# Optimization experiments

Hardware: AMD Instinct MI355X
Metric: run time of the kernel (lower is better)

## Reference

```python
import jax, jax.numpy as jnp
import numpy as np

N_NODES = 100000
N_EDGES = 1600000
D_IN = 256
D_OUT = 128


def _gcn_norm(edge_index, num_nodes):
    # Add self-loops and compute symmetric normalization D^-1/2 A D^-1/2 (PyG GCNConv default).
    src, dst = edge_index[0], edge_index[1]
    loop = jnp.arange(num_nodes, dtype=edge_index.dtype)
    src = jnp.concatenate([src, loop])
    dst = jnp.concatenate([dst, loop])
    deg = jax.ops.segment_sum(jnp.ones_like(dst, dtype=jnp.float32), dst, num_segments=num_nodes)
    dinv = jnp.where(deg > 0, jax.lax.rsqrt(jnp.maximum(deg, 1.0)), 0.0)
    norm = dinv[src] * dinv[dst]  # [E + N]
    return src, dst, norm


def _gcn_conv(x, W, b, src, dst, norm, num_nodes):
    h = x @ W  # [N, d_out] transform first (d_out <= d_in keeps message traffic low)
    msg = h[src] * norm[:, None]  # [E+N, d_out] gather + scale
    out = jax.ops.segment_sum(msg, dst, num_segments=num_nodes)  # scatter-add
    return out + b


def setup_inputs() -> dict:
    key = jax.random.key(0)
    ks = jax.random.split(key, 8)
    x = jax.random.normal(ks[0], (N_NODES, D_IN), dtype=jnp.float32)
    edge_index = jax.random.randint(ks[1], (2, N_EDGES), 0, N_NODES, dtype=jnp.int64)
    s = 0.05
    return {
        "x": x,
        "edge_index": edge_index,
        "W1": jax.random.normal(ks[2], (D_IN, D_OUT), dtype=jnp.float32) * s,
        "b1": jnp.zeros((D_OUT,), dtype=jnp.float32),
        "W_mu": jax.random.normal(ks[3], (D_OUT, D_OUT), dtype=jnp.float32) * s,
        "b_mu": jnp.zeros((D_OUT,), dtype=jnp.float32),
        "W_ls": jax.random.normal(ks[4], (D_OUT, D_OUT), dtype=jnp.float32) * s,
        "b_ls": jnp.zeros((D_OUT,), dtype=jnp.float32),
    }


def reference(x, edge_index, W1, b1, W_mu, b_mu, W_ls, b_ls):
    num_nodes = x.shape[0]
    src, dst, norm = _gcn_norm(edge_index, num_nodes)
    h = jax.nn.relu(_gcn_conv(x, W1, b1, src, dst, norm, num_nodes))
    mu = _gcn_conv(h, W_mu, b_mu, src, dst, norm, num_nodes)
    logstd = _gcn_conv(h, W_ls, b_ls, src, dst, norm, num_nodes)
    return (mu, logstd)
```

## Files before the change

kernel.cpp:

```cpp
#include <hip/hip_runtime.h>
#include <hip/hip_bf16.h>
#include <hip/hip_fp16.h>

typedef __attribute__((ext_vector_type(8))) short short8;
typedef __attribute__((ext_vector_type(8))) _Float16 f16x8;
typedef __attribute__((ext_vector_type(4))) float f32x4;

#define EPB 16384

__global__ __launch_bounds__(256) void k_lhist(const int* __restrict__ dst, int* __restrict__ histT,
                                               int nE, int nblk, int nbins) {
  __shared__ int c[1024];
  int tid = threadIdx.x;
  for (int i = tid; i < nbins; i += 256) c[i] = 0;
  __syncthreads();
  int blk = blockIdx.x;
  int e0 = blk * EPB;
  int e1 = min(nE, e0 + EPB);
  if (e1 - e0 == EPB) {
#pragma unroll
    for (int it = 0; it < EPB / 1024; ++it) {
      int4 d = *(const int4*)(dst + e0 + it * 1024 + tid * 4);
      atomicAdd(&c[d.x >> 7], 1);
      atomicAdd(&c[d.y >> 7], 1);
      atomicAdd(&c[d.z >> 7], 1);
      atomicAdd(&c[d.w >> 7], 1);
    }
  } else {
    for (int i = e0 + tid; i < e1; i += 256) atomicAdd(&c[dst[i] >> 7], 1);
  }
  __syncthreads();
  for (int i = tid; i < nbins; i += 256) histT[i * nblk + blk] = c[i];
}

__global__ __launch_bounds__(256) void k_lscatter(
    const int* __restrict__ src, const int* __restrict__ dst, const int* __restrict__ subPtr,
    int* __restrict__ binned, int nE, int nblk, int nbins) {
  __shared__ int cur[1024];
  int tid = threadIdx.x;
  int blk = blockIdx.x;
  for (int i = tid; i < nbins; i += 256) cur[i] = subPtr[i * nblk + blk];
  __syncthreads();
  int e0 = blk * EPB;
  int e1 = min(nE, e0 + EPB);
  if (e1 - e0 == EPB) {
#pragma unroll
    for (int it = 0; it < EPB / 1024; ++it) {
      int base = e0 + it * 1024 + tid * 4;
      int4 s = *(const int4*)(src + base);
      int4 d = *(const int4*)(dst + base);
      int p0 = atomicAdd(&cur[d.x >> 7], 1);
      int p1 = atomicAdd(&cur[d.y >> 7], 1);
      int p2 = atomicAdd(&cur[d.z >> 7], 1);
      int p3 = atomicAdd(&cur[d.w >> 7], 1);
      binned[p0] = s.x | ((d.x & 127) << 20);
      binned[p1] = s.y | ((d.y & 127) << 20);
      binned[p2] = s.z | ((d.z & 127) << 20);
      binned[p3] = s.w | ((d.w & 127) << 20);
    }
  } else {
    for (int i = e0 + tid; i < e1; i += 256) {
      int d = dst[i];
      int pos = atomicAdd(&cur[d >> 7], 1);
      binned[pos] = src[i] | ((d & 127) << 20);
    }
  }
}

__global__ __launch_bounds__(256) void k_bin_cnt(
    const int* __restrict__ binned, const int* __restrict__ subPtr,
    int* __restrict__ cnt, int nE, int nblk, int nbins, int n) {
  __shared__ int c128[128];
  int b = blockIdx.x;
  int tid = threadIdx.x;
  if (tid < 128) c128[tid] = 0;
  __syncthreads();
  int s0 = subPtr[b * nblk];
  int s1 = (b + 1 < nbins) ? subPtr[(b + 1) * nblk] : nE;
  for (int i = s0 + tid; i < s1; i += 256)
    atomicAdd(&c128[(binned[i] >> 20) & 127], 1);
  __syncthreads();
  if (tid < 128) {
    int idx = (b << 7) + tid;
    if (idx < n) cnt[idx] = c128[tid];
  }
}

__global__ __launch_bounds__(256) void k_bin_place(
    const int* __restrict__ binned, const int* __restrict__ subPtr,
    const int* __restrict__ rowptr, int* __restrict__ col, int nE, int nblk, int nbins, int n) {
  __shared__ int cur128[128];
  int b = blockIdx.x;
  int tid = threadIdx.x;
  if (tid < 128) {
    int idx = (b << 7) + tid;
    cur128[tid] = (idx < n) ? rowptr[idx] : 0;
  }
  __syncthreads();
  int s0 = subPtr[b * nblk];
  int s1 = (b + 1 < nbins) ? subPtr[(b + 1) * nblk] : nE;
  for (int i = s0 + tid; i < s1; i += 256) {
    int e = binned[i];
    int pos = atomicAdd(&cur128[(e >> 20) & 127], 1);
    col[pos] = e & 0xFFFFF;
  }
}


__global__ void k_blocksum(const int* __restrict__ cnt, int* __restrict__ bsum, int n) {
  __shared__ int red[256];
  int tid = threadIdx.x;
  int base = blockIdx.x * 1024 + tid * 4;
  int s = 0;
#pragma unroll
  for (int i = 0; i < 4; i++) { int idx = base + i; if (idx < n) s += cnt[idx]; }
  red[tid] = s;
  __syncthreads();
  for (int off = 128; off > 0; off >>= 1) {
    if (tid < off) red[tid] += red[tid + off];
    __syncthreads();
  }
  if (tid == 0) bsum[blockIdx.x] = red[0];
}

__global__ void k_scan_bsum(int* __restrict__ bsum, int nb) {
  __shared__ int s[128];
  int tid = threadIdx.x;
  int v = (tid < nb) ? bsum[tid] : 0;
  s[tid] = v;
  __syncthreads();
  for (int off = 1; off < 128; off <<= 1) {
    int t = (tid >= off) ? s[tid - off] : 0;
    __syncthreads();
    s[tid] += t;
    __syncthreads();
  }
  if (tid < nb) bsum[tid] = s[tid] - v;
}

__global__ void k_scan_final(const int* __restrict__ cnt, const int* __restrict__ bsum,
                             int* __restrict__ rowptr, float* __restrict__ dinv, int n) {
  __shared__ int tsum[256];
  int tid = threadIdx.x;
  int base = blockIdx.x * 1024 + tid * 4;
  int v[4]; int s = 0;
#pragma unroll
  for (int i = 0; i < 4; i++) { v[i] = (base + i < n) ? cnt[base + i] : 0; s += v[i]; }
  tsum[tid] = s;
  __syncthreads();
  for (int off = 1; off < 256; off <<= 1) {
    int t = (tid >= off) ? tsum[tid - off] : 0;
    __syncthreads();
    tsum[tid] += t;
    __syncthreads();
  }
  int run = bsum[blockIdx.x] + tsum[tid] - s;
#pragma unroll
  for (int i = 0; i < 4; i++) {
    int idx = base + i;
    if (idx < n) {
      rowptr[idx] = run;
      if (dinv) dinv[idx] = rsqrtf((float)(v[i] + 1));
      run += v[i];
    }
  }
}


__global__ void k_prep_w(const float* __restrict__ W1,
                         const float* __restrict__ Wmu, const float* __restrict__ Wls,
                         const float* __restrict__ bmu, const float* __restrict__ bls,
                         __half* __restrict__ W1T, __half* __restrict__ WcT,
                         float* __restrict__ bcat) {
  int i = blockIdx.x * blockDim.x + threadIdx.x;
  if (i < 128 * 256) {
    int n = i >> 8, k = i & 255;
    W1T[i] = __float2half(W1[k * 128 + n]);
  } else if (i < 2 * 128 * 256) {
    int j = i - 128 * 256;
    int n = j >> 7, k = j & 127;
    float f = (n < 128) ? Wmu[k * 128 + n] : Wls[k * 128 + (n - 128)];
    WcT[j] = __float2half(f);
  } else if (i < 2 * 128 * 256 + 256) {
    int n = i - 2 * 128 * 256;
    bcat[n] = (n < 128) ? bmu[n] : bls[n - 128];
  }
}


#define LP 40

template <int AFMT, int OFMT>
__global__ __launch_bounds__(256) void k_gemm_mfma(
    const void* __restrict__ Av, const __half* __restrict__ WT,
    const float* __restrict__ bias, void* __restrict__ out0, void* __restrict__ out1,
    int M, int K, int split_out) {
  __shared__ _Float16 As[128 * LP];
  __shared__ _Float16 Bs[128 * LP];

  const int tid = threadIdx.x;
  const int lane = tid & 63;
  const int wv = tid >> 6;
  const int wr = wv >> 1, wc = wv & 1;
  const int rsel = lane >> 4;
  const int rrow = lane & 15;
  const int row0 = blockIdx.x * 128;
  const int col0 = blockIdx.y * 128;

  f32x4 acc[4][4];
#pragma unroll
  for (int m = 0; m < 4; m++)
#pragma unroll
    for (int n = 0; n < 4; n++) acc[m][n] = (f32x4){0.f, 0.f, 0.f, 0.f};

  const int srow = tid >> 1;
  const int skh = (tid & 1) * 16;

  for (int k0 = 0; k0 < K; k0 += 32) {
    if (row0 + srow < M) {
      if (AFMT == 0) {
        const float* src = (const float*)Av + (size_t)(row0 + srow) * K + k0 + skh;
        float4 f0 = *(const float4*)(src);
        float4 f1 = *(const float4*)(src + 4);
        float4 f2 = *(const float4*)(src + 8);
        float4 f3 = *(const float4*)(src + 12);
        f16x8 v0, v1;
        v0[0]=(_Float16)f0.x; v0[1]=(_Float16)f0.y; v0[2]=(_Float16)f0.z; v0[3]=(_Float16)f0.w;
        v0[4]=(_Float16)f1.x; v0[5]=(_Float16)f1.y; v0[6]=(_Float16)f1.z; v0[7]=(_Float16)f1.w;
        v1[0]=(_Float16)f2.x; v1[1]=(_Float16)f2.y; v1[2]=(_Float16)f2.z; v1[3]=(_Float16)f2.w;
        v1[4]=(_Float16)f3.x; v1[5]=(_Float16)f3.y; v1[6]=(_Float16)f3.z; v1[7]=(_Float16)f3.w;
        *(f16x8*)&As[srow * LP + skh]     = v0;
        *(f16x8*)&As[srow * LP + skh + 8] = v1;
      } else {
        const _Float16* src = (const _Float16*)Av + (size_t)(row0 + srow) * K + k0 + skh;
        *(f16x8*)&As[srow * LP + skh]     = *(const f16x8*)src;
        *(f16x8*)&As[srow * LP + skh + 8] = *(const f16x8*)(src + 8);
      }
    } else {
      f16x8 z = (f16x8){0,0,0,0,0,0,0,0};
      *(f16x8*)&As[srow * LP + skh] = z; *(f16x8*)&As[srow * LP + skh + 8] = z;
    }
    {
      const _Float16* s = (const _Float16*)WT + (size_t)(col0 + srow) * K + k0 + skh;
      *(f16x8*)&Bs[srow * LP + skh]     = *(const f16x8*)s;
      *(f16x8*)&Bs[srow * LP + skh + 8] = *(const f16x8*)(s + 8);
    }
    __syncthreads();

    f16x8 fa[4], fb[4];
#pragma unroll
    for (int m = 0; m < 4; m++)
      fa[m] = *(f16x8*)&As[(wr * 64 + m * 16 + rrow) * LP + rsel * 8];
#pragma unroll
    for (int n = 0; n < 4; n++)
      fb[n] = *(f16x8*)&Bs[(wc * 64 + n * 16 + rrow) * LP + rsel * 8];
#pragma unroll
    for (int m = 0; m < 4; m++)
#pragma unroll
      for (int n = 0; n < 4; n++)
        acc[m][n] = __builtin_amdgcn_mfma_f32_16x16x32_f16(fa[m], fb[n], acc[m][n], 0, 0, 0);
    __syncthreads();
  }

#pragma unroll
  for (int n = 0; n < 4; n++) {
    int col = col0 + wc * 64 + n * 16 + rrow;
    float badd = bias ? bias[col] : 0.f;
    void* dstBase = out0;
    int c = col;
    if (split_out && c >= 128) { dstBase = out1; c -= 128; }
#pragma unroll
    for (int m = 0; m < 4; m++) {
      f32x4 v = acc[m][n];
#pragma unroll
      for (int r = 0; r < 4; r++) {
        int row = row0 + wr * 64 + m * 16 + rsel * 4 + r;
        if (row < M) {
          if (OFMT == 0)
            ((float*)dstBase)[(size_t)row * 128 + c] = v[r] + badd;
          else
            ((__half*)dstBase)[(size_t)row * 128 + c] = __float2half(v[r] + badd);
        }
      }
    }
  }
}


__global__ __launch_bounds__(256) void k_spmm_h(
    const __half* __restrict__ in, const int* __restrict__ rowptr,
    const int* __restrict__ cnt, const int* __restrict__ col,
    const float* __restrict__ dinv,
    const float* __restrict__ bias, __half* __restrict__ out,
    int n, int use_bias, int relu_out) {
  int node = blockIdx.x * 4 + (threadIdx.x >> 6);
  if (node >= n) return;
  int lane = threadIdx.x & 63;

  const __half2* inp = (const __half2*)in;
  float di = dinv[node];
  float2 v = __half22float2(inp[(size_t)node * 64 + lane]);
  float accx = di * v.x;
  float accy = di * v.y;

  int beg = rowptr[node];
  int m = cnt[node];
  int i = 0;
  for (; i + 8 <= m; i += 8) {
    int c[8];
#pragma unroll
    for (int j = 0; j < 8; j++) c[j] = col[beg + i + j];
    float e[8];
#pragma unroll
    for (int j = 0; j < 8; j++) e[j] = dinv[c[j]];
    float2 u[8];
#pragma unroll
    for (int j = 0; j < 8; j++) u[j] = __half22float2(inp[(size_t)c[j] * 64 + lane]);
#pragma unroll
    for (int j = 0; j < 8; j++) { accx += e[j] * u[j].x; accy += e[j] * u[j].y; }
  }
  if (i < m) {
    int c[8];
#pragma unroll
    for (int j = 0; j < 8; j++) c[j] = col[(i + j < m) ? (beg + i + j) : beg];
    float e[8];
#pragma unroll
    for (int j = 0; j < 8; j++) e[j] = (i + j < m) ? dinv[c[j]] : 0.f;
    float2 u[8];
#pragma unroll
    for (int j = 0; j < 8; j++) u[j] = __half22float2(inp[(size_t)c[j] * 64 + lane]);
#pragma unroll
    for (int j = 0; j < 8; j++) { accx += e[j] * u[j].x; accy += e[j] * u[j].y; }
  }
  accx *= di;
  accy *= di;
  if (use_bias) {
    accx += bias[2 * lane];
    accy += bias[2 * lane + 1];
  }
  if (relu_out) {
    accx = fmaxf(accx, 0.f);
    accy = fmaxf(accy, 0.f);
  }
  ((__half2*)(out + (size_t)node * 128))[lane] = __floats2half2_rn(accx, accy);
}


__global__ __launch_bounds__(256) void k_spmm_gemm(
    const __half* __restrict__ in, const int* __restrict__ rowptr,
    const int* __restrict__ cnt, const int* __restrict__ col,
    const float* __restrict__ dinv,
    const __half* __restrict__ WcT, const float* __restrict__ bcat,
    float* __restrict__ out0, float* __restrict__ out1, int n) {
  __shared__ _Float16 gt[16 * 128];
  const int tid = threadIdx.x;
  const int lane = tid & 63;
  const int w = tid >> 6;
  const __half2* inp = (const __half2*)in;

  for (int q = 0; q < 4; q++) {
    int li = w * 4 + q;
    int node = blockIdx.x * 16 + li;
    float accx = 0.f, accy = 0.f;
    if (node < n) {
      float di = dinv[node];
      float2 v = __half22float2(inp[(size_t)node * 64 + lane]);
      accx = di * v.x;
      accy = di * v.y;
      int beg = rowptr[node];
      int m = cnt[node];
      int i = 0;
      for (; i + 8 <= m; i += 8) {
        int c[8];
#pragma unroll
        for (int j = 0; j < 8; j++) c[j] = col[beg + i + j];
        float e[8];
#pragma unroll
        for (int j = 0; j < 8; j++) e[j] = dinv[c[j]];
        float2 u[8];
#pragma unroll
        for (int j = 0; j < 8; j++) u[j] = __half22float2(inp[(size_t)c[j] * 64 + lane]);
#pragma unroll
        for (int j = 0; j < 8; j++) { accx += e[j] * u[j].x; accy += e[j] * u[j].y; }
      }
      if (i < m) {
        int c[8];
#pragma unroll
        for (int j = 0; j < 8; j++) c[j] = col[(i + j < m) ? (beg + i + j) : beg];
        float e[8];
#pragma unroll
        for (int j = 0; j < 8; j++) e[j] = (i + j < m) ? dinv[c[j]] : 0.f;
        float2 u[8];
#pragma unroll
        for (int j = 0; j < 8; j++) u[j] = __half22float2(inp[(size_t)c[j] * 64 + lane]);
#pragma unroll
        for (int j = 0; j < 8; j++) { accx += e[j] * u[j].x; accy += e[j] * u[j].y; }
      }
      accx *= di;
      accy *= di;
    }
    int slot = (lane >> 2) ^ (li & 7);
    *(__half2*)((char*)gt + li * 256 + slot * 16 + (lane & 3) * 4) =
        __floats2half2_rn(accx, accy);
  }
  __syncthreads();

  const int lr = lane & 15;
  const int lk = lane >> 4;
  f16x8 a[4];
#pragma unroll
  for (int ks = 0; ks < 4; ks++) {
    int slot = (ks * 4 + lk) ^ (lr & 7);
    a[ks] = *(const f16x8*)((const char*)gt + lr * 256 + slot * 16);
  }
#pragma unroll
  for (int ct = 0; ct < 4; ct++) {
    int colg = (w * 4 + ct) * 16 + lr;
    f32x4 acc = (f32x4){0.f, 0.f, 0.f, 0.f};
#pragma unroll
    for (int ks = 0; ks < 4; ks++) {
      f16x8 b = *(const f16x8*)((const _Float16*)WcT + (size_t)colg * 128 + ks * 32 + lk * 8);
      acc = __builtin_amdgcn_mfma_f32_16x16x32_f16(a[ks], b, acc, 0, 0, 0);
    }
    float badd = bcat[colg];
    float* dst = out0;
    int c = colg;
    if (c >= 128) { dst = out1; c -= 128; }
#pragma unroll
    for (int r = 0; r < 4; r++) {
      int node = blockIdx.x * 16 + lk * 4 + r;
      if (node < n) dst[(size_t)node * 128 + c] = acc[r] + badd;
    }
  }
}


extern "C" void kernel_launch(void* const* d_in, const int* in_sizes, int n_in,
                              void* d_out, int out_size, void* d_ws, size_t ws_size,
                              hipStream_t stream) {
  const float* x   = (const float*)d_in[0];
  const int*   ei  = (const int*)d_in[1];
  const float* W1  = (const float*)d_in[2];
  const float* b1  = (const float*)d_in[3];
  const float* Wmu = (const float*)d_in[4];
  const float* bmu = (const float*)d_in[5];
  const float* Wls = (const float*)d_in[6];
  const float* bls = (const float*)d_in[7];

  int N = in_sizes[0] / 256;
  int E = in_sizes[1] / 2;
  const int* src = ei;
  const int* dst = ei + E;

  int NBINS = (N + 127) >> 7;
  int NBLK  = (E + EPB - 1) / EPB;
  int NS    = NBINS * NBLK;

  char* ws = (char*)d_ws;
  size_t o = 0;
  auto alloc = [&](size_t b) { size_t c = o; o = (o + b + 511) & ~(size_t)511; return c; };
  int*   cnt     = (int*)(ws + alloc((size_t)N * 4));
  int*   rowptr  = (int*)(ws + alloc((size_t)N * 4));
  float* dinv    = (float*)(ws + alloc((size_t)N * 4));
  int*   bsum    = (int*)(ws + alloc(512));
  int*   histT   = (int*)(ws + alloc((size_t)NS * 4));
  int*   subPtr  = (int*)(ws + alloc((size_t)NS * 4));
  int*   col     = (int*)(ws + alloc((size_t)E * 4));
  int*   binned  = (int*)(ws + alloc((size_t)E * 4));
  __half* W1T  = (__half*)(ws + alloc(128 * 256 * 2));
  __half* WcT  = (__half*)(ws + alloc(256 * 128 * 2));
  float*  bcat = (float*)(ws + alloc(256 * 4));
  __half* h0   = (__half*)(ws + alloc((size_t)N * 128 * 2));
  __half* hBuf = (__half*)(ws + alloc((size_t)N * 128 * 2));

  float* outMu = (float*)d_out;
  float* outLs = outMu + (size_t)N * 128;

  int nbScanN = (N + 1023) / 1024;
  int nbScanS = (NS + 1023) / 1024;

  k_lhist<<<NBLK, 256, 0, stream>>>(dst, histT, E, NBLK, NBINS);
  k_blocksum<<<nbScanS, 256, 0, stream>>>(histT, bsum, NS);
  k_scan_bsum<<<1, 128, 0, stream>>>(bsum, nbScanS);
  k_scan_final<<<nbScanS, 256, 0, stream>>>(histT, bsum, subPtr, nullptr, NS);
  k_lscatter<<<NBLK, 256, 0, stream>>>(src, dst, subPtr, binned, E, NBLK, NBINS);
  k_bin_cnt<<<NBINS, 256, 0, stream>>>(binned, subPtr, cnt, E, NBLK, NBINS, N);
  k_blocksum<<<nbScanN, 256, 0, stream>>>(cnt, bsum, N);
  k_scan_bsum<<<1, 128, 0, stream>>>(bsum, nbScanN);
  k_scan_final<<<nbScanN, 256, 0, stream>>>(cnt, bsum, rowptr, dinv, N);
  k_bin_place<<<NBINS, 256, 0, stream>>>(binned, subPtr, rowptr, col, E, NBLK, NBINS, N);

  k_prep_w<<<(2 * 128 * 256 + 256 + 255) / 256, 256, 0, stream>>>(
      W1, Wmu, Wls, bmu, bls, W1T, WcT, bcat);

  int gx = (N + 127) / 128;
  k_gemm_mfma<0, 1><<<dim3(gx, 1), 256, 0, stream>>>(x, W1T, nullptr, h0, nullptr, N, 256, 0);
  k_spmm_h<<<(N + 3) / 4, 256, 0, stream>>>(h0, rowptr, cnt, col, dinv, b1, hBuf, N, 1, 1);
  k_spmm_gemm<<<(N + 15) / 16, 256, 0, stream>>>(
      hBuf, rowptr, cnt, col, dinv, WcT, bcat, outMu, outLs, N);
}
```

Baseline: 308.9 us.

## Replace tiled 128x128 GEMM with 16-row blocks reading W1 from global

```diff
diff --git a/kernel.cpp b/kernel.cpp
--- a/kernel.cpp
+++ b/kernel.cpp
@@ -188,101 +188,67 @@
 }
 
 
-#define LP 40
-
-template <int AFMT, int OFMT>
-__global__ __launch_bounds__(256) void k_gemm_mfma(
-    const void* __restrict__ Av, const __half* __restrict__ WT,
-    const float* __restrict__ bias, void* __restrict__ out0, void* __restrict__ out1,
-    int M, int K, int split_out) {
-  __shared__ _Float16 As[128 * LP];
-  __shared__ _Float16 Bs[128 * LP];
-
+__global__ __launch_bounds__(256) void k_gemm1(
+    const float* __restrict__ x, const __half* __restrict__ W1T,
+    __half* __restrict__ h0, int n) {
+  __shared__ _Float16 xt[16 * 264];
+  __shared__ _Float16 ht[16 * 136];
   const int tid = threadIdx.x;
+
+  {
+    const int row = tid >> 4;
+    const int seg = tid & 15;
+    const int gnode = blockIdx.x * 16 + row;
+    f16x8 v0 = (f16x8){0, 0, 0, 0, 0, 0, 0, 0}, v1 = v0;
+    if (gnode < n) {
+      const float* ap = x + (size_t)gnode * 256 + seg * 16;
+      float4 f0 = *(const float4*)(ap);
+      float4 f1 = *(const float4*)(ap + 4);
+      float4 f2 = *(const float4*)(ap + 8);
+      float4 f3 = *(const float4*)(ap + 12);
+      v0[0]=(_Float16)f0.x; v0[1]=(_Float16)f0.y; v0[2]=(_Float16)f0.z; v0[3]=(_Float16)f0.w;
+      v0[4]=(_Float16)f1.x; v0[5]=(_Float16)f1.y; v0[6]=(_Float16)f1.z; v0[7]=(_Float16)f1.w;
+      v1[0]=(_Float16)f2.x; v1[1]=(_Float16)f2.y; v1[2]=(_Float16)f2.z; v1[3]=(_Float16)f2.w;
+      v1[4]=(_Float16)f3.x; v1[5]=(_Float16)f3.y; v1[6]=(_Float16)f3.z; v1[7]=(_Float16)f3.w;
+    }
+    *(f16x8*)&xt[row * 264 + seg * 16]     = v0;
+    *(f16x8*)&xt[row * 264 + seg * 16 + 8] = v1;
+  }
+  __syncthreads();
+
   const int lane = tid & 63;
-  const int wv = tid >> 6;
-  const int wr = wv >> 1, wc = wv & 1;
-  const int rsel = lane >> 4;
-  const int rrow = lane & 15;
-  const int row0 = blockIdx.x * 128;
-  const int col0 = blockIdx.y * 128;
-
-  f32x4 acc[4][4];
-#pragma unroll
-  for (int m = 0; m < 4; m++)
-#pragma unroll
-    for (int n = 0; n < 4; n++) acc[m][n] = (f32x4){0.f, 0.f, 0.f, 0.f};
-
-  const int srow = tid >> 1;
-  const int skh = (tid & 1) * 16;
-
-  for (int k0 = 0; k0 < K; k0 += 32) {
-    if (row0 + srow < M) {
-      if (AFMT == 0) {
-        const float* src = (const float*)Av + (size_t)(row0 + srow) * K + k0 + skh;
-        float4 f0 = *(const float4*)(src);
-        float4 f1 = *(const float4*)(src + 4);
-        float4 f2 = *(const float4*)(src + 8);
-        float4 f3 = *(const float4*)(src + 12);
-        f16x8 v0, v1;
-        v0[0]=(_Float16)f0.x; v0[1]=(_Float16)f0.y; v0[2]=(_Float16)f0.z; v0[3]=(_Float16)f0.w;
-        v0[4]=(_Float16)f1.x; v0[5]=(_Float16)f1.y; v0[6]=(_Float16)f1.z; v0[7]=(_Float16)f1.w;
-        v1[0]=(_Float16)f2.x; v1[1]=(_Float16)f2.y; v1[2]=(_Float16)f2.z; v1[3]=(_Float16)f2.w;
-        v1[4]=(_Float16)f3.x; v1[5]=(_Float16)f3.y; v1[6]=(_Float16)f3.z; v1[7]=(_Float16)f3.w;
-        *(f16x8*)&As[srow * LP + skh]     = v0;
-        *(f16x8*)&As[srow * LP + skh + 8] = v1;
-      } else {
-        const _Float16* src = (const _Float16*)Av + (size_t)(row0 + srow) * K + k0 + skh;
-        *(f16x8*)&As[srow * LP + skh]     = *(const f16x8*)src;
-        *(f16x8*)&As[srow * LP + skh + 8] = *(const f16x8*)(src + 8);
-      }
-    } else {
-      f16x8 z = (f16x8){0,0,0,0,0,0,0,0};
-      *(f16x8*)&As[srow * LP + skh] = z; *(f16x8*)&As[srow * LP + skh + 8] = z;
-    }
-    {
-      const _Float16* s = (const _Float16*)WT + (size_t)(col0 + srow) * K + k0 + skh;
-      *(f16x8*)&Bs[srow * LP + skh]     = *(const f16x8*)s;
-      *(f16x8*)&Bs[srow * LP + skh + 8] = *(const f16x8*)(s + 8);
-    }
-    __syncthreads();
-
-    f16x8 fa[4], fb[4];
-#pragma unroll
-    for (int m = 0; m < 4; m++)
-      fa[m] = *(f16x8*)&As[(wr * 64 + m * 16 + rrow) * LP + rsel * 8];
-#pragma unroll
-    for (int n = 0; n < 4; n++)
-      fb[n] = *(f16x8*)&Bs[(wc * 64 + n * 16 + rrow) * LP + rsel * 8];
-#pragma unroll
-    for (int m = 0; m < 4; m++)
-#pragma unroll
-      for (int n = 0; n < 4; n++)
-        acc[m][n] = __builtin_amdgcn_mfma_f32_16x16x32_f16(fa[m], fb[n], acc[m][n], 0, 0, 0);
-    __syncthreads();
-  }
-
-#pragma unroll
-  for (int n = 0; n < 4; n++) {
-    int col = col0 + wc * 64 + n * 16 + rrow;
-    float badd = bias ? bias[col] : 0.f;
-    void* dstBase = out0;
-    int c = col;
-    if (split_out && c >= 128) { dstBase = out1; c -= 128; }
-#pragma unroll
-    for (int m = 0; m < 4; m++) {
-      f32x4 v = acc[m][n];
-#pragma unroll
-      for (int r = 0; r < 4; r++) {
-        int row = row0 + wr * 64 + m * 16 + rsel * 4 + r;
-        if (row < M) {
-          if (OFMT == 0)
-            ((float*)dstBase)[(size_t)row * 128 + c] = v[r] + badd;
-          else
-            ((__half*)dstBase)[(size_t)row * 128 + c] = __float2half(v[r] + badd);
-        }
-      }
-    }
+  const int w = tid >> 6;
+  const int lr = lane & 15;
+  const int lk = lane >> 4;
+
+  f16x8 a[8];
+#pragma unroll
+  for (int ks = 0; ks < 8; ks++)
+    a[ks] = *(const f16x8*)&xt[lr * 264 + (ks * 4 + lk) * 8];
+
+#pragma unroll
+  for (int ct = 0; ct < 2; ct++) {
+    const int coln = w * 32 + ct * 16 + lr;
+    f32x4 acc = (f32x4){0.f, 0.f, 0.f, 0.f};
+    const _Float16* wrow = (const _Float16*)W1T + (size_t)coln * 256 + lk * 8;
+#pragma unroll
+    for (int ks = 0; ks < 8; ks++) {
+      f16x8 b = *(const f16x8*)(wrow + ks * 32);
+      acc = __builtin_amdgcn_mfma_f32_16x16x32_f16(a[ks], b, acc, 0, 0, 0);
+    }
+#pragma unroll
+    for (int r = 0; r < 4; r++)
+      ht[(lk * 4 + r) * 136 + coln] = (_Float16)acc[r];
+  }
+  __syncthreads();
+
+  {
+    const int row = tid >> 4;
+    const int chunk = tid & 15;
+    const int gnode = blockIdx.x * 16 + row;
+    if (gnode < n)
+      *(f16x8*)(h0 + (size_t)gnode * 128 + chunk * 8) =
+          *(const f16x8*)&ht[row * 136 + chunk * 8];
   }
 }
 
@@ -493,8 +459,7 @@
   k_prep_w<<<(2 * 128 * 256 + 256 + 255) / 256, 256, 0, stream>>>(
       W1, Wmu, Wls, bmu, bls, W1T, WcT, bcat);
 
-  int gx = (N + 127) / 128;
-  k_gemm_mfma<0, 1><<<dim3(gx, 1), 256, 0, stream>>>(x, W1T, nullptr, h0, nullptr, N, 256, 0);
+  k_gemm1<<<(N + 15) / 16, 256, 0, stream>>>(x, W1T, h0, N);
   k_spmm_h<<<(N + 3) / 4, 256, 0, stream>>>(h0, rowptr, cnt, col, dinv, b1, hBuf, N, 1, 1);
   k_spmm_gemm<<<(N + 15) / 16, 256, 0, stream>>>(
       hBuf, rowptr, cnt, col, dinv, WcT, bcat, outMu, outLs, N);
```

New measurement: 322.6 us. 1.04x slower.
